# Performance work log

Measured on AMD Instinct MI355X. Metric: run time of the kernel, lower is better.

Reference implementation:

```python
import jax, jax.numpy as jnp
import numpy as np

H, D, TS, A, R, TR = 256, 2, 32, 4, 16, 8  # h_size, max_output_degree, t_size, n_aggr, rank, t_rank
BS = 16384


def setup_inputs() -> dict:
    key = jax.random.key(0)
    ks = jax.random.split(key, 9)
    return {
        "neighbour_h": jax.random.normal(ks[0], (BS, D, H), jnp.float32),
        "type_embs": jax.random.normal(ks[1], (BS, TS), jnp.float32),
        # per-child input projections U: (max_output_degree, n_aggr, h_size, rank)
        "U": jax.random.normal(ks[2], (D, A, H, R), jnp.float32) * 0.05,
        "b": jax.random.normal(ks[3], (D, A, 1, R), jnp.float32) * 0.05,
        # type projection
        "U_type": jax.random.normal(ks[4], (TS, A * TR), jnp.float32) * 0.05,
        "b_type": jax.random.normal(ks[5], (1, A * TR), jnp.float32) * 0.05,
        # stacked augmented core tensors T_list: (n_aggr, t_rank+1, rank+1, rank+1, rank)
        "T": jax.random.normal(ks[6], (A, TR + 1, R + 1, R + 1, R), jnp.float32) * 0.02,
        # output projection
        "U_output": jax.random.normal(ks[7], (A, R, H), jnp.float32) * 0.05,
        "b_output": jax.random.normal(ks[8], (A, 1, H), jnp.float32) * 0.05,
    }


def _aug(x):
    # append a constant-1 feature along the last dim: (bs, a, d) -> (bs, a, d+1)
    bs, a, _ = x.shape
    return jnp.concatenate([x, jnp.ones((bs, a, 1), x.dtype)], axis=-1)


def reference(neighbour_h, type_embs, U, b, U_type, b_type, T, U_output, b_output):
    # child projections: (bs, n_ch, n_aggr, rank)
    ch = jnp.einsum('bch,cahr->bcar', neighbour_h, U) + b[:, :, 0, :]
    # type projection: (bs, n_aggr, t_rank)
    tp = (type_embs @ U_type + b_type).reshape(-1, A, TR)
    # augmented (homogeneous) inputs
    h0 = _aug(tp)         # (bs, a, TR+1)
    h1 = _aug(ch[:, 0])   # (bs, a, R+1)
    h2 = _aug(ch[:, 1])   # (bs, a, R+1)
    # sequential multilinear (Tucker/HOSVD) contraction with the core tensor,
    # vectorized over batch and aggregators (original loops over n_aggr)
    r = jnp.einsum('bap,apqrs->baqrs', h0, T)
    r = jnp.einsum('baq,baqrs->bars', h1, r)
    g = jnp.einsum('bar,bars->bas', h2, r)            # (bs, a, R)
    out = jnp.einsum('bar,arh->bah', g, U_output) + b_output[:, 0, :]
    return out.reshape(neighbour_h.shape[0], -1)      # (bs, n_aggr*h_size)
```

## Files before the change

### kernel.cpp

```cpp
#include <hip/hip_runtime.h>

#define NTHR 512
#define TB 32

typedef __attribute__((ext_vector_type(8))) short bf16x8;
typedef __attribute__((ext_vector_type(4))) float f32x4;
typedef float4 f4;
typedef unsigned short u16;

__device__ __forceinline__ u16 f2b(float x) {
  union { float f; unsigned u; } v; v.f = x;
  unsigned r = (v.u + 0x7fffu + ((v.u >> 16) & 1u)) >> 16;
  return (u16)r;
}
__device__ __forceinline__ float b2f(u16 u) {
  union { unsigned u; float f; } v; v.u = ((unsigned)u) << 16;
  return v.f;
}
__device__ __forceinline__ unsigned pack2(float a, float b) {
  return (unsigned)f2b(a) | ((unsigned)f2b(b) << 16);
}
__device__ __forceinline__ unsigned cvtpk(float lo, float hi) {
  unsigned r;
  asm("v_cvt_pk_bf16_f32 %0, %1, %2" : "=v"(r) : "v"(lo), "v"(hi));
  return r;
}

extern "C" __global__ void hosvd_prep(const float* __restrict__ U,
                                      const float* __restrict__ T,
                                      const float* __restrict__ UO,
                                      unsigned* __restrict__ ws32) {
  int id = blockIdx.x * 256 + threadIdx.x;
  if (id < 92160) {
    int j2 = id & 3, frag = id >> 2;
    int l = frag & 63, f2 = frag >> 6;
    int p = f2 % 9, akt = f2 / 9;
    int kt = akt % 10, a = akt / 10;
    int s = l & 15;
    float v[2];
    #pragma unroll
    for (int j = 0; j < 2; ++j) {
      int kp = kt * 32 + (l >> 4) * 8 + j2 * 2 + j;
      float x = 0.f;
      if (kp < 306) {
        int q = (unsigned)kp / 18u, r = kp - q * 18;
        if (r < 17) x = T[(((a * 9 + p) * 17 + q) * 17 + r) * 16 + s];
      }
      v[j] = x;
    }
    ws32[id] = pack2(v[0], v[1]);
  } else if (id < 108544) {
    int rel = id - 92160;
    int j2 = rel & 3, frag = rel >> 2;
    int l = frag & 63, f2 = frag >> 6;
    int kt = f2 & 7, g = f2 >> 3;
    int a = g & 3, c = g >> 2;
    int rr = l & 15;
    int k = kt * 32 + (l >> 4) * 8 + j2 * 2;
    float v0 = U[((c * 4 + a) * 256 + k + 0) * 16 + rr];
    float v1 = U[((c * 4 + a) * 256 + k + 1) * 16 + rr];
    ws32[id] = pack2(v0, v1);
  } else if (id < 124928) {
    int rel = id - 108544;
    int j2 = rel & 3, frag = rel >> 2;
    int l = frag & 63, f2 = frag >> 6;
    int ht = f2 & 15, a = f2 >> 4;
    int h = ht * 16 + (l & 15);
    int k = (l >> 4) * 8 + j2 * 2;
    float v0 = (k + 0 < 16) ? UO[(a * 16 + k + 0) * 256 + h] : 0.f;
    float v1 = (k + 1 < 16) ? UO[(a * 16 + k + 1) * 256 + h] : 0.f;
    ws32[id] = pack2(v0, v1);
  }
}

#define MFMA_B(A, B, C) __builtin_amdgcn_mfma_f32_16x16x32_bf16(A, B, C, 0, 0, 0)

extern "C" __global__ __launch_bounds__(NTHR, 4)
void hosvd_main(const float* __restrict__ nh, const float* __restrict__ te,
                const float* __restrict__ bw, const float* __restrict__ Ut,
                const float* __restrict__ bt, const float* __restrict__ bO,
                const u16* __restrict__ BTf, const u16* __restrict__ UcTf,
                const u16* __restrict__ UOTf, float* __restrict__ out) {
  __shared__ __align__(16) u16   s_u[18688];
  __shared__ __align__(16) u16   s_ch[TB * 164];
  __shared__ __align__(16) float s_tpt[36 * 32];
  __shared__ __align__(16) u16   s_g[TB * 136];

  const int t = threadIdx.x;
  const int ib0 = blockIdx.x * TB;
  const int w = t >> 6, l = t & 63;
  const int rl = l & 15, q = l >> 4;

  float* teL = (float*)s_g;
  float* UtL = (float*)&s_u[16640];

  if (t < 256) {
    const int row = t >> 3, cc = (t >> 2) & 1, aa = t & 3;
    *(uint2*)&s_ch[row * 164 + cc * 80 + aa * 20 + 16] = make_uint2(0x3F80u, 0u);
  }
  if (t < 128) {
    const int aa = t >> 5, row = t & 31;
    s_tpt[(aa * 9 + 8) * 32 + row] = 1.0f;
  }

  if (t < 256) {
    const int row = t >> 3, k4 = t & 7;
    f4 v = *(const f4*)&te[(size_t)(ib0 + row) * 32 + k4 * 4];
    float* d = &teL[row * 33 + k4 * 4];
    d[0] = v.x; d[1] = v.y; d[2] = v.z; d[3] = v.w;
  } else {
    const int j = t - 256;
    *(f4*)&UtL[j * 4] = *(const f4*)&Ut[j * 4];
  }
  for (int lp = t; lp < 4096; lp += NTHR) {
    const int row = lp >> 7, rem = lp & 127;
    const int c = rem >> 6, k0 = (rem & 63) * 4;
    f4 v = *(const f4*)&nh[((size_t)(ib0 + row) * 2 + c) * 256 + k0];
    *(uint2*)&s_u[row * 520 + c * 256 + k0] =
        make_uint2(cvtpk(v.x, v.y), cvtpk(v.z, v.w));
  }
  __syncthreads();

  {
    const int i = t >> 4, o = t & 15;
    const int off = o * 2;
    const int aa = off >> 3, p0 = off & 7;
    float acc0 = bt[off], acc1 = bt[off + 1];
    #pragma unroll
    for (int k = 0; k < 32; ++k) {
      float tv = teL[i * 33 + k];
      float2 u = *(const float2*)&UtL[k * 32 + off];
      acc0 = fmaf(tv, u.x, acc0);
      acc1 = fmaf(tv, u.y, acc1);
    }
    s_tpt[(aa * 9 + p0) * 32 + i]     = acc0;
    s_tpt[(aa * 9 + p0 + 1) * 32 + i] = acc1;
  }

  {
    const int c = w >> 2, a = w & 3;
    const u16* u0 = &UcTf[((size_t)((c * 4 + a) * 8) * 64 + l) * 8];
    bf16x8 C0 = *(const bf16x8*)(u0 + 0 * 512);
    bf16x8 C1 = *(const bf16x8*)(u0 + 1 * 512);
    bf16x8 C2 = *(const bf16x8*)(u0 + 2 * 512);
    bf16x8 C3 = *(const bf16x8*)(u0 + 3 * 512);
    bf16x8 C4 = *(const bf16x8*)(u0 + 4 * 512);
    bf16x8 C5 = *(const bf16x8*)(u0 + 5 * 512);
    bf16x8 C6 = *(const bf16x8*)(u0 + 6 * 512);
    bf16x8 C7 = *(const bf16x8*)(u0 + 7 * 512);
    f32x4 ac0 = {0.f, 0.f, 0.f, 0.f}, ac1 = {0.f, 0.f, 0.f, 0.f};
    #define PCKT(KT, CB)                                                          \
    {                                                                             \
      bf16x8 A0_ = *(const bf16x8*)&s_u[rl * 520 + c * 256 + KT * 32 + 8 * q];    \
      bf16x8 A1_ = *(const bf16x8*)&s_u[(16 + rl) * 520 + c * 256 + KT * 32 + 8 * q]; \
      ac0 = MFMA_B(A0_, CB, ac0);                                                 \
      ac1 = MFMA_B(A1_, CB, ac1);                                                 \
    }
    PCKT(0, C0) PCKT(1, C1) PCKT(2, C2) PCKT(3, C3)
    PCKT(4, C4) PCKT(5, C5) PCKT(6, C6) PCKT(7, C7)
    #undef PCKT
    const float bias = bw[(c * 4 + a) * 16 + rl];
    #pragma unroll
    for (int reg = 0; reg < 4; ++reg) {
      s_ch[(4 * q + reg) * 164 + c * 80 + a * 20 + rl]      = f2b(ac0[reg] + bias);
      s_ch[(16 + 4 * q + reg) * 164 + c * 80 + a * 20 + rl] = f2b(ac1[reg] + bias);
    }
  }
  __syncthreads();

  {
    const int a = w & 3, m = w >> 2;
    const int row = m * 16 + rl;
    const u16* h1g = &s_ch[row * 164 + a * 20];
    const u16* h2g = &s_ch[row * 164 + 80 + a * 20];

    f32x4 acc[9];
    #pragma unroll
    for (int p = 0; p < 9; ++p) acc[p] = (f32x4){0.f, 0.f, 0.f, 0.f};

    __builtin_amdgcn_s_setprio(1);
    #pragma unroll
    for (int kt = 0; kt < 10; ++kt) {
      const u16* bp = &BTf[(size_t)((a * 10 + kt) * 9) * 512 + l * 8];
      bf16x8 B0 = *(const bf16x8*)(bp + 0 * 512);
      bf16x8 B1 = *(const bf16x8*)(bp + 1 * 512);
      bf16x8 B2 = *(const bf16x8*)(bp + 2 * 512);
      bf16x8 B3 = *(const bf16x8*)(bp + 3 * 512);
      bf16x8 B4 = *(const bf16x8*)(bp + 4 * 512);
      bf16x8 B5 = *(const bf16x8*)(bp + 5 * 512);
      bf16x8 B6 = *(const bf16x8*)(bp + 6 * 512);
      bf16x8 B7 = *(const bf16x8*)(bp + 7 * 512);
      bf16x8 B8 = *(const bf16x8*)(bp + 8 * 512);

      const int k0 = kt * 32 + 8 * q;
      const unsigned qq0 = (unsigned)k0 / 18u;
      const int rr0 = k0 - (int)qq0 * 18;
      const int brk = 18 - rr0;
      const float h1a = b2f(h1g[qq0]);
      const float h1b = b2f(h1g[qq0 + 1]);
      float hv[8];
      #pragma unroll
      for (int j = 0; j < 8; ++j) {
        int rr = rr0 + j;
        rr = (rr >= 18) ? rr - 18 : rr;
        const float h2v = b2f(h2g[rr]);
        const float h1v = (j < brk) ? h1a : h1b;
        hv[j] = h1v * h2v;
      }
      union { unsigned u[4]; bf16x8 v; } Au;
      Au.u[0] = cvtpk(hv[0], hv[1]);
      Au.u[1] = cvtpk(hv[2], hv[3]);
      Au.u[2] = cvtpk(hv[4], hv[5]);
      Au.u[3] = cvtpk(hv[6], hv[7]);

      acc[0] = MFMA_B(Au.v, B0, acc[0]);
      acc[1] = MFMA_B(Au.v, B1, acc[1]);
      acc[2] = MFMA_B(Au.v, B2, acc[2]);
      acc[3] = MFMA_B(Au.v, B3, acc[3]);
      acc[4] = MFMA_B(Au.v, B4, acc[4]);
      acc[5] = MFMA_B(Au.v, B5, acc[5]);
      acc[6] = MFMA_B(Au.v, B6, acc[6]);
      acc[7] = MFMA_B(Au.v, B7, acc[7]);
      acc[8] = MFMA_B(Au.v, B8, acc[8]);
    }
    __builtin_amdgcn_s_setprio(0);

    float gp[4] = {0.f, 0.f, 0.f, 0.f};
    #pragma unroll
    for (int p = 0; p < 9; ++p) {
      f4 tv = *(const f4*)&s_tpt[(a * 9 + p) * 32 + m * 16 + 4 * q];
      gp[0] = fmaf(tv.x, acc[p][0], gp[0]);
      gp[1] = fmaf(tv.y, acc[p][1], gp[1]);
      gp[2] = fmaf(tv.z, acc[p][2], gp[2]);
      gp[3] = fmaf(tv.w, acc[p][3], gp[3]);
    }
    #pragma unroll
    for (int reg = 0; reg < 4; ++reg) {
      const int row2 = m * 16 + 4 * q + reg;
      s_g[row2 * 136 + a * 32 + rl]      = f2b(gp[reg]);
      s_g[row2 * 136 + a * 32 + 16 + rl] = 0;
    }
  }
  __syncthreads();

  {
    const int e = w;
    #pragma unroll
    for (int a = 0; a < 4; ++a) {
      const u16* ub = &UOTf[((size_t)(a * 16 + e * 2) * 64 + l) * 8];
      bf16x8 E0 = *(const bf16x8*)(ub);
      bf16x8 E1 = *(const bf16x8*)(ub + 512);
      bf16x8 A0 = *(const bf16x8*)&s_g[rl * 136 + a * 32 + 8 * q];
      bf16x8 A1 = *(const bf16x8*)&s_g[(16 + rl) * 136 + a * 32 + 8 * q];
      const float b0 = bO[a * 256 + (e * 2 + 0) * 16 + rl];
      const float b1 = bO[a * 256 + (e * 2 + 1) * 16 + rl];
      f32x4 e00 = {b0, b0, b0, b0}, e01 = e00;
      f32x4 e10 = {b1, b1, b1, b1}, e11 = e10;
      e00 = MFMA_B(A0, E0, e00);
      e01 = MFMA_B(A1, E0, e01);
      e10 = MFMA_B(A0, E1, e10);
      e11 = MFMA_B(A1, E1, e11);
      #pragma unroll
      for (int reg = 0; reg < 4; ++reg) {
        const size_t r0 = (size_t)(ib0 + 4 * q + reg) * 1024 + a * 256;
        const size_t r1 = (size_t)(ib0 + 16 + 4 * q + reg) * 1024 + a * 256;
        out[r0 + (e * 2 + 0) * 16 + rl] = e00[reg];
        out[r1 + (e * 2 + 0) * 16 + rl] = e01[reg];
        out[r0 + (e * 2 + 1) * 16 + rl] = e10[reg];
        out[r1 + (e * 2 + 1) * 16 + rl] = e11[reg];
      }
    }
  }
}

extern "C" void kernel_launch(void* const* d_in, const int* in_sizes, int n_in,
                              void* d_out, int out_size, void* d_ws, size_t ws_size,
                              hipStream_t stream) {
  const float* nh = (const float*)d_in[0];
  const float* te = (const float*)d_in[1];
  const float* U  = (const float*)d_in[2];
  const float* bw = (const float*)d_in[3];
  const float* Ut = (const float*)d_in[4];
  const float* bt = (const float*)d_in[5];
  const float* T  = (const float*)d_in[6];
  const float* UO = (const float*)d_in[7];
  const float* bO = (const float*)d_in[8];
  float* out = (float*)d_out;

  unsigned* ws32 = (unsigned*)d_ws;
  hipLaunchKernelGGL(hosvd_prep, dim3(488), dim3(256), 0, stream, U, T, UO, ws32);

  const u16* BTf  = (const u16*)d_ws;
  const u16* UcTf = BTf + 184320;
  const u16* UOTf = UcTf + 32768;

  const int bs = in_sizes[0] / 512;
  hipLaunchKernelGGL(hosvd_main, dim3(bs / TB), dim3(NTHR), 0, stream,
                     nh, te, bw, Ut, bt, bO, BTf, UcTf, UOTf, out);
}
```

Before: 41.49 us.

## Switch all GEMM stages to 32x32x16 MFMA with split-K core contraction

Re-lays out the prepared weight fragments for the 32x32x16 bf16 MFMA shape and rewrites the child projection, core-tensor contraction and output projection to use it. The core contraction now splits K across two wave groups and reduces the partial sums through shared memory plus a lane shuffle. The child projection runs on four waves while the other four compute the type projection concurrently. The intent is fewer MFMA issues and better operand reuse per instruction. In exchange it adds zero-padding work on the N dimension (the last tile uses the padded p index), an extra fp32 reduction through LDS, and larger shared memory use.

```diff
diff --git a/kernel.cpp b/kernel.cpp
--- a/kernel.cpp
+++ b/kernel.cpp
@@ -4,7 +4,7 @@
 #define TB 32
 
 typedef __attribute__((ext_vector_type(8))) short bf16x8;
-typedef __attribute__((ext_vector_type(4))) float f32x4;
+typedef __attribute__((ext_vector_type(16))) float f32x16;
 typedef float4 f4;
 typedef unsigned short u16;
 
@@ -25,55 +25,55 @@
   asm("v_cvt_pk_bf16_f32 %0, %1, %2" : "=v"(r) : "v"(lo), "v"(hi));
   return r;
 }
+
+#define MFMA32(A, B, C) __builtin_amdgcn_mfma_f32_32x32x16_bf16(A, B, C, 0, 0, 0)
 
 extern "C" __global__ void hosvd_prep(const float* __restrict__ U,
                                       const float* __restrict__ T,
                                       const float* __restrict__ UO,
                                       unsigned* __restrict__ ws32) {
   int id = blockIdx.x * 256 + threadIdx.x;
-  if (id < 92160) {
+  if (id < 102400) {
     int j2 = id & 3, frag = id >> 2;
     int l = frag & 63, f2 = frag >> 6;
-    int p = f2 % 9, akt = f2 / 9;
-    int kt = akt % 10, a = akt / 10;
-    int s = l & 15;
+    int nt = f2 % 5, aks = f2 / 5;
+    int ks = aks % 20, a = aks / 20;
+    int n = nt * 32 + (l & 31);
+    int p = n >> 4, s = n & 15;
     float v[2];
     #pragma unroll
     for (int j = 0; j < 2; ++j) {
-      int kp = kt * 32 + (l >> 4) * 8 + j2 * 2 + j;
+      int kp = ks * 16 + (l >> 5) * 8 + j2 * 2 + j;
+      int q = (unsigned)kp / 18u, r = kp - q * 18;
       float x = 0.f;
-      if (kp < 306) {
-        int q = (unsigned)kp / 18u, r = kp - q * 18;
-        if (r < 17) x = T[(((a * 9 + p) * 17 + q) * 17 + r) * 16 + s];
-      }
+      if (p <= 8 && q <= 16 && r <= 16)
+        x = T[(((a * 9 + p) * 17 + q) * 17 + r) * 16 + s];
       v[j] = x;
     }
     ws32[id] = pack2(v[0], v[1]);
-  } else if (id < 108544) {
-    int rel = id - 92160;
+  } else if (id < 118784) {
+    int rel = id - 102400;
     int j2 = rel & 3, frag = rel >> 2;
     int l = frag & 63, f2 = frag >> 6;
-    int kt = f2 & 7, g = f2 >> 3;
-    int a = g & 3, c = g >> 2;
-    int rr = l & 15;
-    int k = kt * 32 + (l >> 4) * 8 + j2 * 2;
+    int nt = f2 & 1, ks = (f2 >> 1) & 15, c = f2 >> 5;
+    int n = nt * 32 + (l & 31);
+    int a = n >> 4, rr = n & 15;
+    int k = ks * 16 + (l >> 5) * 8 + j2 * 2;
     float v0 = U[((c * 4 + a) * 256 + k + 0) * 16 + rr];
     float v1 = U[((c * 4 + a) * 256 + k + 1) * 16 + rr];
     ws32[id] = pack2(v0, v1);
-  } else if (id < 124928) {
-    int rel = id - 108544;
+  } else if (id < 126976) {
+    int rel = id - 118784;
     int j2 = rel & 3, frag = rel >> 2;
     int l = frag & 63, f2 = frag >> 6;
-    int ht = f2 & 15, a = f2 >> 4;
-    int h = ht * 16 + (l & 15);
-    int k = (l >> 4) * 8 + j2 * 2;
-    float v0 = (k + 0 < 16) ? UO[(a * 16 + k + 0) * 256 + h] : 0.f;
-    float v1 = (k + 1 < 16) ? UO[(a * 16 + k + 1) * 256 + h] : 0.f;
+    int ht = f2 & 7, a = f2 >> 3;
+    int h = ht * 32 + (l & 31);
+    int k = (l >> 5) * 8 + j2 * 2;
+    float v0 = UO[(a * 16 + k + 0) * 256 + h];
+    float v1 = UO[(a * 16 + k + 1) * 256 + h];
     ws32[id] = pack2(v0, v1);
   }
 }
-
-#define MFMA_B(A, B, C) __builtin_amdgcn_mfma_f32_16x16x32_bf16(A, B, C, 0, 0, 0)
 
 extern "C" __global__ __launch_bounds__(NTHR, 4)
 void hosvd_main(const float* __restrict__ nh, const float* __restrict__ te,
@@ -81,18 +81,18 @@
                 const float* __restrict__ bt, const float* __restrict__ bO,
                 const u16* __restrict__ BTf, const u16* __restrict__ UcTf,
                 const u16* __restrict__ UOTf, float* __restrict__ out) {
-  __shared__ __align__(16) u16   s_u[18688];
+  __shared__ __align__(16) u16   s_u[20800];
   __shared__ __align__(16) u16   s_ch[TB * 164];
   __shared__ __align__(16) float s_tpt[36 * 32];
-  __shared__ __align__(16) u16   s_g[TB * 136];
 
   const int t = threadIdx.x;
   const int ib0 = blockIdx.x * TB;
   const int w = t >> 6, l = t & 63;
-  const int rl = l & 15, q = l >> 4;
-
-  float* teL = (float*)s_g;
+  const int l31 = l & 31, hi = l >> 5;
+
   float* UtL = (float*)&s_u[16640];
+  float* teL = (float*)&s_u[18688];
+  float* s_redf = (float*)s_u;
 
   if (t < 256) {
     const int row = t >> 3, cc = (t >> 2) & 1, aa = t & 3;
@@ -121,91 +121,82 @@
   }
   __syncthreads();
 
+  if (w < 4) {
+    const int c = w & 1, nt2 = w >> 1;
+    f32x16 accC = {0.f, 0.f, 0.f, 0.f, 0.f, 0.f, 0.f, 0.f,
+                   0.f, 0.f, 0.f, 0.f, 0.f, 0.f, 0.f, 0.f};
+    #pragma unroll
+    for (int ks = 0; ks < 16; ++ks) {
+      bf16x8 Av = *(const bf16x8*)&s_u[l31 * 520 + c * 256 + ks * 16 + hi * 8];
+      bf16x8 Bv = *(const bf16x8*)
+          &UcTf[(size_t)(((c * 16 + ks) * 2 + nt2) * 64 + l) * 8];
+      accC = MFMA32(Av, Bv, accC);
+    }
+    const int n = nt2 * 32 + l31;
+    const int ca = n >> 4, rr = n & 15;
+    const float bias = bw[(c * 4 + ca) * 16 + rr];
+    #pragma unroll
+    for (int reg = 0; reg < 16; ++reg) {
+      const int row = (reg & 3) + 8 * (reg >> 2) + 4 * hi;
+      s_ch[row * 164 + c * 80 + ca * 20 + rr] = f2b(accC[reg] + bias);
+    }
+  } else {
+    const int t2 = t - 256;
+    const int i = t2 >> 3, off = (t2 & 7) * 4;
+    float ac0 = bt[off], ac1 = bt[off + 1], ac2 = bt[off + 2], ac3 = bt[off + 3];
+    #pragma unroll
+    for (int k = 0; k < 32; ++k) {
+      const float tv = teL[i * 33 + k];
+      f4 u = *(const f4*)&UtL[k * 32 + off];
+      ac0 = fmaf(tv, u.x, ac0);
+      ac1 = fmaf(tv, u.y, ac1);
+      ac2 = fmaf(tv, u.z, ac2);
+      ac3 = fmaf(tv, u.w, ac3);
+    }
+    #pragma unroll
+    for (int jj = 0; jj < 4; ++jj) {
+      const int o2 = off + jj;
+      const float v = (jj == 0) ? ac0 : (jj == 1) ? ac1 : (jj == 2) ? ac2 : ac3;
+      s_tpt[((o2 >> 3) * 9 + (o2 & 7)) * 32 + i] = v;
+    }
+  }
+  __syncthreads();
+
   {
-    const int i = t >> 4, o = t & 15;
-    const int off = o * 2;
-    const int aa = off >> 3, p0 = off & 7;
-    float acc0 = bt[off], acc1 = bt[off + 1];
-    #pragma unroll
-    for (int k = 0; k < 32; ++k) {
-      float tv = teL[i * 33 + k];
-      float2 u = *(const float2*)&UtL[k * 32 + off];
-      acc0 = fmaf(tv, u.x, acc0);
-      acc1 = fmaf(tv, u.y, acc1);
-    }
-    s_tpt[(aa * 9 + p0) * 32 + i]     = acc0;
-    s_tpt[(aa * 9 + p0 + 1) * 32 + i] = acc1;
-  }
-
-  {
-    const int c = w >> 2, a = w & 3;
-    const u16* u0 = &UcTf[((size_t)((c * 4 + a) * 8) * 64 + l) * 8];
-    bf16x8 C0 = *(const bf16x8*)(u0 + 0 * 512);
-    bf16x8 C1 = *(const bf16x8*)(u0 + 1 * 512);
-    bf16x8 C2 = *(const bf16x8*)(u0 + 2 * 512);
-    bf16x8 C3 = *(const bf16x8*)(u0 + 3 * 512);
-    bf16x8 C4 = *(const bf16x8*)(u0 + 4 * 512);
-    bf16x8 C5 = *(const bf16x8*)(u0 + 5 * 512);
-    bf16x8 C6 = *(const bf16x8*)(u0 + 6 * 512);
-    bf16x8 C7 = *(const bf16x8*)(u0 + 7 * 512);
-    f32x4 ac0 = {0.f, 0.f, 0.f, 0.f}, ac1 = {0.f, 0.f, 0.f, 0.f};
-    #define PCKT(KT, CB)                                                          \
-    {                                                                             \
-      bf16x8 A0_ = *(const bf16x8*)&s_u[rl * 520 + c * 256 + KT * 32 + 8 * q];    \
-      bf16x8 A1_ = *(const bf16x8*)&s_u[(16 + rl) * 520 + c * 256 + KT * 32 + 8 * q]; \
-      ac0 = MFMA_B(A0_, CB, ac0);                                                 \
-      ac1 = MFMA_B(A1_, CB, ac1);                                                 \
-    }
-    PCKT(0, C0) PCKT(1, C1) PCKT(2, C2) PCKT(3, C3)
-    PCKT(4, C4) PCKT(5, C5) PCKT(6, C6) PCKT(7, C7)
-    #undef PCKT
-    const float bias = bw[(c * 4 + a) * 16 + rl];
-    #pragma unroll
-    for (int reg = 0; reg < 4; ++reg) {
-      s_ch[(4 * q + reg) * 164 + c * 80 + a * 20 + rl]      = f2b(ac0[reg] + bias);
-      s_ch[(16 + 4 * q + reg) * 164 + c * 80 + a * 20 + rl] = f2b(ac1[reg] + bias);
-    }
-  }
-  __syncthreads();
-
-  {
-    const int a = w & 3, m = w >> 2;
-    const int row = m * 16 + rl;
-    const u16* h1g = &s_ch[row * 164 + a * 20];
-    const u16* h2g = &s_ch[row * 164 + 80 + a * 20];
-
-    f32x4 acc[9];
-    #pragma unroll
-    for (int p = 0; p < 9; ++p) acc[p] = (f32x4){0.f, 0.f, 0.f, 0.f};
+    const int a = w & 3, kh = w >> 2;
+    const u16* h1g = &s_ch[l31 * 164 + a * 20];
+    const u16* h2g = h1g + 80;
+
+    f32x16 acc[5];
+    #pragma unroll
+    for (int nt = 0; nt < 5; ++nt)
+      acc[nt] = (f32x16){0.f, 0.f, 0.f, 0.f, 0.f, 0.f, 0.f, 0.f,
+                         0.f, 0.f, 0.f, 0.f, 0.f, 0.f, 0.f, 0.f};
 
     __builtin_amdgcn_s_setprio(1);
     #pragma unroll
-    for (int kt = 0; kt < 10; ++kt) {
-      const u16* bp = &BTf[(size_t)((a * 10 + kt) * 9) * 512 + l * 8];
+    for (int ks2 = 0; ks2 < 10; ++ks2) {
+      const int ks = kh * 10 + ks2;
+      const u16* bp = &BTf[(size_t)((a * 20 + ks) * 5) * 512 + l * 8];
       bf16x8 B0 = *(const bf16x8*)(bp + 0 * 512);
       bf16x8 B1 = *(const bf16x8*)(bp + 1 * 512);
       bf16x8 B2 = *(const bf16x8*)(bp + 2 * 512);
       bf16x8 B3 = *(const bf16x8*)(bp + 3 * 512);
       bf16x8 B4 = *(const bf16x8*)(bp + 4 * 512);
-      bf16x8 B5 = *(const bf16x8*)(bp + 5 * 512);
-      bf16x8 B6 = *(const bf16x8*)(bp + 6 * 512);
-      bf16x8 B7 = *(const bf16x8*)(bp + 7 * 512);
-      bf16x8 B8 = *(const bf16x8*)(bp + 8 * 512);
-
-      const int k0 = kt * 32 + 8 * q;
-      const unsigned qq0 = (unsigned)k0 / 18u;
-      const int rr0 = k0 - (int)qq0 * 18;
-      const int brk = 18 - rr0;
-      const float h1a = b2f(h1g[qq0]);
-      const float h1b = b2f(h1g[qq0 + 1]);
+
+      const int k0 = ks * 16 + hi * 8;
+      const unsigned q0 = (unsigned)k0 / 18u;
+      const int r0 = k0 - (int)q0 * 18;
+      const int brk = 18 - r0;
+      const float h1a = b2f(h1g[q0]);
+      const float h1b = b2f(h1g[q0 + 1]);
       float hv[8];
       #pragma unroll
       for (int j = 0; j < 8; ++j) {
-        int rr = rr0 + j;
+        int rr = r0 + j;
         rr = (rr >= 18) ? rr - 18 : rr;
         const float h2v = b2f(h2g[rr]);
-        const float h1v = (j < brk) ? h1a : h1b;
-        hv[j] = h1v * h2v;
+        hv[j] = ((j < brk) ? h1a : h1b) * h2v;
       }
       union { unsigned u[4]; bf16x8 v; } Au;
       Au.u[0] = cvtpk(hv[0], hv[1]);
@@ -213,61 +204,79 @@
       Au.u[2] = cvtpk(hv[4], hv[5]);
       Au.u[3] = cvtpk(hv[6], hv[7]);
 
-      acc[0] = MFMA_B(Au.v, B0, acc[0]);
-      acc[1] = MFMA_B(Au.v, B1, acc[1]);
-      acc[2] = MFMA_B(Au.v, B2, acc[2]);
-      acc[3] = MFMA_B(Au.v, B3, acc[3]);
-      acc[4] = MFMA_B(Au.v, B4, acc[4]);
-      acc[5] = MFMA_B(Au.v, B5, acc[5]);
-      acc[6] = MFMA_B(Au.v, B6, acc[6]);
-      acc[7] = MFMA_B(Au.v, B7, acc[7]);
-      acc[8] = MFMA_B(Au.v, B8, acc[8]);
+      acc[0] = MFMA32(Au.v, B0, acc[0]);
+      acc[1] = MFMA32(Au.v, B1, acc[1]);
+      acc[2] = MFMA32(Au.v, B2, acc[2]);
+      acc[3] = MFMA32(Au.v, B3, acc[3]);
+      acc[4] = MFMA32(Au.v, B4, acc[4]);
     }
     __builtin_amdgcn_s_setprio(0);
 
-    float gp[4] = {0.f, 0.f, 0.f, 0.f};
-    #pragma unroll
-    for (int p = 0; p < 9; ++p) {
-      f4 tv = *(const f4*)&s_tpt[(a * 9 + p) * 32 + m * 16 + 4 * q];
-      gp[0] = fmaf(tv.x, acc[p][0], gp[0]);
-      gp[1] = fmaf(tv.y, acc[p][1], gp[1]);
-      gp[2] = fmaf(tv.z, acc[p][2], gp[2]);
-      gp[3] = fmaf(tv.w, acc[p][3], gp[3]);
-    }
-    #pragma unroll
-    for (int reg = 0; reg < 4; ++reg) {
-      const int row2 = m * 16 + 4 * q + reg;
-      s_g[row2 * 136 + a * 32 + rl]      = f2b(gp[reg]);
-      s_g[row2 * 136 + a * 32 + 16 + rl] = 0;
+    float gp[16];
+    #pragma unroll
+    for (int reg = 0; reg < 16; ++reg) gp[reg] = 0.f;
+    #pragma unroll
+    for (int nt = 0; nt < 5; ++nt) {
+      int pp = nt * 2 + (l31 >> 4);
+      if (pp > 8) pp = 8;
+      const float* tpb = &s_tpt[(a * 9 + pp) * 32 + 4 * hi];
+      f4 t0 = *(const f4*)&tpb[0];
+      f4 t1 = *(const f4*)&tpb[8];
+      f4 t2 = *(const f4*)&tpb[16];
+      f4 t3 = *(const f4*)&tpb[24];
+      gp[0]  = fmaf(t0.x, acc[nt][0],  gp[0]);
+      gp[1]  = fmaf(t0.y, acc[nt][1],  gp[1]);
+      gp[2]  = fmaf(t0.z, acc[nt][2],  gp[2]);
+      gp[3]  = fmaf(t0.w, acc[nt][3],  gp[3]);
+      gp[4]  = fmaf(t1.x, acc[nt][4],  gp[4]);
+      gp[5]  = fmaf(t1.y, acc[nt][5],  gp[5]);
+      gp[6]  = fmaf(t1.z, acc[nt][6],  gp[6]);
+      gp[7]  = fmaf(t1.w, acc[nt][7],  gp[7]);
+      gp[8]  = fmaf(t2.x, acc[nt][8],  gp[8]);
+      gp[9]  = fmaf(t2.y, acc[nt][9],  gp[9]);
+      gp[10] = fmaf(t2.z, acc[nt][10], gp[10]);
+      gp[11] = fmaf(t2.w, acc[nt][11], gp[11]);
+      gp[12] = fmaf(t3.x, acc[nt][12], gp[12]);
+      gp[13] = fmaf(t3.y, acc[nt][13], gp[13]);
+      gp[14] = fmaf(t3.z, acc[nt][14], gp[14]);
+      gp[15] = fmaf(t3.w, acc[nt][15], gp[15]);
+    }
+    #pragma unroll
+    for (int reg = 0; reg < 16; ++reg)
+      gp[reg] += __shfl_xor(gp[reg], 16, 64);
+    if ((l & 16) == 0) {
+      const int s = l & 15;
+      #pragma unroll
+      for (int reg = 0; reg < 16; ++reg) {
+        const int row = (reg & 3) + 8 * (reg >> 2) + 4 * hi;
+        s_redf[((kh * 4 + a) * 32 + row) * 16 + s] = gp[reg];
+      }
     }
   }
   __syncthreads();
 
   {
-    const int e = w;
     #pragma unroll
     for (int a = 0; a < 4; ++a) {
-      const u16* ub = &UOTf[((size_t)(a * 16 + e * 2) * 64 + l) * 8];
-      bf16x8 E0 = *(const bf16x8*)(ub);
-      bf16x8 E1 = *(const bf16x8*)(ub + 512);
-      bf16x8 A0 = *(const bf16x8*)&s_g[rl * 136 + a * 32 + 8 * q];
-      bf16x8 A1 = *(const bf16x8*)&s_g[(16 + rl) * 136 + a * 32 + 8 * q];
-      const float b0 = bO[a * 256 + (e * 2 + 0) * 16 + rl];
-      const float b1 = bO[a * 256 + (e * 2 + 1) * 16 + rl];
-      f32x4 e00 = {b0, b0, b0, b0}, e01 = e00;
-      f32x4 e10 = {b1, b1, b1, b1}, e11 = e10;
-      e00 = MFMA_B(A0, E0, e00);
-      e01 = MFMA_B(A1, E0, e01);
-      e10 = MFMA_B(A0, E1, e10);
-      e11 = MFMA_B(A1, E1, e11);
+      const float* r0p = &s_redf[((0 + a) * 32 + l31) * 16 + hi * 8];
+      const float* r1p = &s_redf[((4 + a) * 32 + l31) * 16 + hi * 8];
+      f4 xa = *(const f4*)&r0p[0], xb = *(const f4*)&r0p[4];
+      f4 ya = *(const f4*)&r1p[0], yb = *(const f4*)&r1p[4];
+      union { unsigned u[4]; bf16x8 v; } Au;
+      Au.u[0] = cvtpk(xa.x + ya.x, xa.y + ya.y);
+      Au.u[1] = cvtpk(xa.z + ya.z, xa.w + ya.w);
+      Au.u[2] = cvtpk(xb.x + yb.x, xb.y + yb.y);
+      Au.u[3] = cvtpk(xb.z + yb.z, xb.w + yb.w);
+      bf16x8 Bv = *(const bf16x8*)&UOTf[((size_t)(a * 8 + w) * 64 + l) * 8];
+      const int h = w * 32 + l31;
+      const float bias = bO[a * 256 + h];
+      f32x16 accE = {bias, bias, bias, bias, bias, bias, bias, bias,
+                     bias, bias, bias, bias, bias, bias, bias, bias};
+      accE = MFMA32(Au.v, Bv, accE);
       #pragma unroll
-      for (int reg = 0; reg < 4; ++reg) {
-        const size_t r0 = (size_t)(ib0 + 4 * q + reg) * 1024 + a * 256;
-        const size_t r1 = (size_t)(ib0 + 16 + 4 * q + reg) * 1024 + a * 256;
-        out[r0 + (e * 2 + 0) * 16 + rl] = e00[reg];
-        out[r1 + (e * 2 + 0) * 16 + rl] = e01[reg];
-        out[r0 + (e * 2 + 1) * 16 + rl] = e10[reg];
-        out[r1 + (e * 2 + 1) * 16 + rl] = e11[reg];
+      for (int reg = 0; reg < 16; ++reg) {
+        const int row = (reg & 3) + 8 * (reg >> 2) + 4 * hi;
+        out[(size_t)(ib0 + row) * 1024 + a * 256 + h] = accE[reg];
       }
     }
   }
@@ -288,10 +297,10 @@
   float* out = (float*)d_out;
 
   unsigned* ws32 = (unsigned*)d_ws;
-  hipLaunchKernelGGL(hosvd_prep, dim3(488), dim3(256), 0, stream, U, T, UO, ws32);
+  hipLaunchKernelGGL(hosvd_prep, dim3(496), dim3(256), 0, stream, U, T, UO, ws32);
 
   const u16* BTf  = (const u16*)d_ws;
-  const u16* UcTf = BTf + 184320;
+  const u16* UcTf = BTf + 204800;
   const u16* UOTf = UcTf + 32768;
 
   const int bs = in_sizes[0] / 512;
```

After: 39.47 us. -4.9%, faster.

## Halve block tile to 16 rows with 256 threads and overlap type projection

Applied to the files above, without the earlier changes.

Shrinks the per-block batch tile from 32 to 16 rows with 256 threads, doubling the grid and cutting LDS use per block so more blocks can be resident. The child projection now runs on two warps, each covering four aggregators with its A fragments held in registers, while the other two warps compute the type projection at the same time. Every warp now handles one aggregator for all 16 rows. Each block reloads the core and projection weights, so weight traffic from global/L2 doubles for the same amount of output.

```diff
diff --git a/kernel.cpp b/kernel.cpp
--- a/kernel.cpp
+++ b/kernel.cpp
@@ -1,7 +1,7 @@
 #include <hip/hip_runtime.h>
 
-#define NTHR 512
-#define TB 32
+#define NTHR 256
+#define TB 16
 
 typedef __attribute__((ext_vector_type(8))) short bf16x8;
 typedef __attribute__((ext_vector_type(4))) float f32x4;
@@ -25,6 +25,8 @@
   asm("v_cvt_pk_bf16_f32 %0, %1, %2" : "=v"(r) : "v"(lo), "v"(hi));
   return r;
 }
+
+#define MFMA_B(A, B, C) __builtin_amdgcn_mfma_f32_16x16x32_bf16(A, B, C, 0, 0, 0)
 
 extern "C" __global__ void hosvd_prep(const float* __restrict__ U,
                                       const float* __restrict__ T,
@@ -73,17 +75,15 @@
   }
 }
 
-#define MFMA_B(A, B, C) __builtin_amdgcn_mfma_f32_16x16x32_bf16(A, B, C, 0, 0, 0)
-
 extern "C" __global__ __launch_bounds__(NTHR, 4)
 void hosvd_main(const float* __restrict__ nh, const float* __restrict__ te,
                 const float* __restrict__ bw, const float* __restrict__ Ut,
                 const float* __restrict__ bt, const float* __restrict__ bO,
                 const u16* __restrict__ BTf, const u16* __restrict__ UcTf,
                 const u16* __restrict__ UOTf, float* __restrict__ out) {
-  __shared__ __align__(16) u16   s_u[18688];
+  __shared__ __align__(16) u16   s_u[11424];
   __shared__ __align__(16) u16   s_ch[TB * 164];
-  __shared__ __align__(16) float s_tpt[36 * 32];
+  __shared__ __align__(16) float s_tpt[36 * 16];
   __shared__ __align__(16) u16   s_g[TB * 136];
 
   const int t = threadIdx.x;
@@ -91,28 +91,26 @@
   const int w = t >> 6, l = t & 63;
   const int rl = l & 15, q = l >> 4;
 
-  float* teL = (float*)s_g;
-  float* UtL = (float*)&s_u[16640];
-
-  if (t < 256) {
+  float* UtL = (float*)&s_u[8320];
+  float* teL = (float*)&s_u[10368];
+
+  if (t < 128) {
     const int row = t >> 3, cc = (t >> 2) & 1, aa = t & 3;
     *(uint2*)&s_ch[row * 164 + cc * 80 + aa * 20 + 16] = make_uint2(0x3F80u, 0u);
   }
+  if (t < 64) {
+    const int aa = t >> 4, row = t & 15;
+    s_tpt[(aa * 9 + 8) * 16 + row] = 1.0f;
+  }
+
   if (t < 128) {
-    const int aa = t >> 5, row = t & 31;
-    s_tpt[(aa * 9 + 8) * 32 + row] = 1.0f;
-  }
-
-  if (t < 256) {
     const int row = t >> 3, k4 = t & 7;
     f4 v = *(const f4*)&te[(size_t)(ib0 + row) * 32 + k4 * 4];
     float* d = &teL[row * 33 + k4 * 4];
     d[0] = v.x; d[1] = v.y; d[2] = v.z; d[3] = v.w;
-  } else {
-    const int j = t - 256;
-    *(f4*)&UtL[j * 4] = *(const f4*)&Ut[j * 4];
-  }
-  for (int lp = t; lp < 4096; lp += NTHR) {
+  }
+  *(f4*)&UtL[t * 4] = *(const f4*)&Ut[t * 4];
+  for (int lp = t; lp < 2048; lp += NTHR) {
     const int row = lp >> 7, rem = lp & 127;
     const int c = rem >> 6, k0 = (rem & 63) * 4;
     f4 v = *(const f4*)&nh[((size_t)(ib0 + row) * 2 + c) * 256 + k0];
@@ -121,58 +119,52 @@
   }
   __syncthreads();
 
+  if (w < 2) {
+    const int c = w;
+    bf16x8 Af[8];
+    #pragma unroll
+    for (int kt = 0; kt < 8; ++kt)
+      Af[kt] = *(const bf16x8*)&s_u[rl * 520 + c * 256 + kt * 32 + 8 * q];
+    #pragma unroll
+    for (int a = 0; a < 4; ++a) {
+      const u16* u0 = &UcTf[((size_t)((c * 4 + a) * 8) * 64 + l) * 8];
+      f32x4 ac = {0.f, 0.f, 0.f, 0.f};
+      #pragma unroll
+      for (int kt = 0; kt < 8; ++kt) {
+        bf16x8 Bv = *(const bf16x8*)(u0 + kt * 512);
+        ac = MFMA_B(Af[kt], Bv, ac);
+      }
+      const float bias = bw[(c * 4 + a) * 16 + rl];
+      #pragma unroll
+      for (int reg = 0; reg < 4; ++reg)
+        s_ch[(4 * q + reg) * 164 + c * 80 + a * 20 + rl] = f2b(ac[reg] + bias);
+    }
+  } else {
+    const int t2 = t - 128;
+    const int i = t2 >> 3, off = (t2 & 7) * 4;
+    float ac0 = bt[off], ac1 = bt[off + 1], ac2 = bt[off + 2], ac3 = bt[off + 3];
+    #pragma unroll
+    for (int k = 0; k < 32; ++k) {
+      const float tv = teL[i * 33 + k];
+      f4 u = *(const f4*)&UtL[k * 32 + off];
+      ac0 = fmaf(tv, u.x, ac0);
+      ac1 = fmaf(tv, u.y, ac1);
+      ac2 = fmaf(tv, u.z, ac2);
+      ac3 = fmaf(tv, u.w, ac3);
+    }
+    #pragma unroll
+    for (int jj = 0; jj < 4; ++jj) {
+      const int o2 = off + jj;
+      const float v = (jj == 0) ? ac0 : (jj == 1) ? ac1 : (jj == 2) ? ac2 : ac3;
+      s_tpt[((o2 >> 3) * 9 + (o2 & 7)) * 16 + i] = v;
+    }
+  }
+  __syncthreads();
+
   {
-    const int i = t >> 4, o = t & 15;
-    const int off = o * 2;
-    const int aa = off >> 3, p0 = off & 7;
-    float acc0 = bt[off], acc1 = bt[off + 1];
-    #pragma unroll
-    for (int k = 0; k < 32; ++k) {
-      float tv = teL[i * 33 + k];
-      float2 u = *(const float2*)&UtL[k * 32 + off];
-      acc0 = fmaf(tv, u.x, acc0);
-      acc1 = fmaf(tv, u.y, acc1);
-    }
-    s_tpt[(aa * 9 + p0) * 32 + i]     = acc0;
-    s_tpt[(aa * 9 + p0 + 1) * 32 + i] = acc1;
-  }
-
-  {
-    const int c = w >> 2, a = w & 3;
-    const u16* u0 = &UcTf[((size_t)((c * 4 + a) * 8) * 64 + l) * 8];
-    bf16x8 C0 = *(const bf16x8*)(u0 + 0 * 512);
-    bf16x8 C1 = *(const bf16x8*)(u0 + 1 * 512);
-    bf16x8 C2 = *(const bf16x8*)(u0 + 2 * 512);
-    bf16x8 C3 = *(const bf16x8*)(u0 + 3 * 512);
-    bf16x8 C4 = *(const bf16x8*)(u0 + 4 * 512);
-    bf16x8 C5 = *(const bf16x8*)(u0 + 5 * 512);
-    bf16x8 C6 = *(const bf16x8*)(u0 + 6 * 512);
-    bf16x8 C7 = *(const bf16x8*)(u0 + 7 * 512);
-    f32x4 ac0 = {0.f, 0.f, 0.f, 0.f}, ac1 = {0.f, 0.f, 0.f, 0.f};
-    #define PCKT(KT, CB)                                                          \
-    {                                                                             \
-      bf16x8 A0_ = *(const bf16x8*)&s_u[rl * 520 + c * 256 + KT * 32 + 8 * q];    \
-      bf16x8 A1_ = *(const bf16x8*)&s_u[(16 + rl) * 520 + c * 256 + KT * 32 + 8 * q]; \
-      ac0 = MFMA_B(A0_, CB, ac0);                                                 \
-      ac1 = MFMA_B(A1_, CB, ac1);                                                 \
-    }
-    PCKT(0, C0) PCKT(1, C1) PCKT(2, C2) PCKT(3, C3)
-    PCKT(4, C4) PCKT(5, C5) PCKT(6, C6) PCKT(7, C7)
-    #undef PCKT
-    const float bias = bw[(c * 4 + a) * 16 + rl];
-    #pragma unroll
-    for (int reg = 0; reg < 4; ++reg) {
-      s_ch[(4 * q + reg) * 164 + c * 80 + a * 20 + rl]      = f2b(ac0[reg] + bias);
-      s_ch[(16 + 4 * q + reg) * 164 + c * 80 + a * 20 + rl] = f2b(ac1[reg] + bias);
-    }
-  }
-  __syncthreads();
-
-  {
-    const int a = w & 3, m = w >> 2;
-    const int row = m * 16 + rl;
-    const u16* h1g = &s_ch[row * 164 + a * 20];
-    const u16* h2g = &s_ch[row * 164 + 80 + a * 20];
+    const int a = w;
+    const u16* h1g = &s_ch[rl * 164 + a * 20];
+    const u16* h2g = h1g + 80;
 
     f32x4 acc[9];
     #pragma unroll
@@ -193,19 +185,18 @@
       bf16x8 B8 = *(const bf16x8*)(bp + 8 * 512);
 
       const int k0 = kt * 32 + 8 * q;
-      const unsigned qq0 = (unsigned)k0 / 18u;
-      const int rr0 = k0 - (int)qq0 * 18;
-      const int brk = 18 - rr0;
-      const float h1a = b2f(h1g[qq0]);
-      const float h1b = b2f(h1g[qq0 + 1]);
+      const unsigned q0 = (unsigned)k0 / 18u;
+      const int r0 = k0 - (int)q0 * 18;
+      const int brk = 18 - r0;
+      const float h1a = b2f(h1g[q0]);
+      const float h1b = b2f(h1g[q0 + 1]);
       float hv[8];
       #pragma unroll
       for (int j = 0; j < 8; ++j) {
-        int rr = rr0 + j;
+        int rr = r0 + j;
         rr = (rr >= 18) ? rr - 18 : rr;
         const float h2v = b2f(h2g[rr]);
-        const float h1v = (j < brk) ? h1a : h1b;
-        hv[j] = h1v * h2v;
+        hv[j] = ((j < brk) ? h1a : h1b) * h2v;
       }
       union { unsigned u[4]; bf16x8 v; } Au;
       Au.u[0] = cvtpk(hv[0], hv[1]);
@@ -228,7 +219,7 @@
     float gp[4] = {0.f, 0.f, 0.f, 0.f};
     #pragma unroll
     for (int p = 0; p < 9; ++p) {
-      f4 tv = *(const f4*)&s_tpt[(a * 9 + p) * 32 + m * 16 + 4 * q];
+      f4 tv = *(const f4*)&s_tpt[(a * 9 + p) * 16 + 4 * q];
       gp[0] = fmaf(tv.x, acc[p][0], gp[0]);
       gp[1] = fmaf(tv.y, acc[p][1], gp[1]);
       gp[2] = fmaf(tv.z, acc[p][2], gp[2]);
@@ -236,7 +227,7 @@
     }
     #pragma unroll
     for (int reg = 0; reg < 4; ++reg) {
-      const int row2 = m * 16 + 4 * q + reg;
+      const int row2 = 4 * q + reg;
       s_g[row2 * 136 + a * 32 + rl]      = f2b(gp[reg]);
       s_g[row2 * 136 + a * 32 + 16 + rl] = 0;
     }
@@ -247,27 +238,18 @@
     const int e = w;
     #pragma unroll
     for (int a = 0; a < 4; ++a) {
-      const u16* ub = &UOTf[((size_t)(a * 16 + e * 2) * 64 + l) * 8];
-      bf16x8 E0 = *(const bf16x8*)(ub);
-      bf16x8 E1 = *(const bf16x8*)(ub + 512);
-      bf16x8 A0 = *(const bf16x8*)&s_g[rl * 136 + a * 32 + 8 * q];
-      bf16x8 A1 = *(const bf16x8*)&s_g[(16 + rl) * 136 + a * 32 + 8 * q];
-      const float b0 = bO[a * 256 + (e * 2 + 0) * 16 + rl];
-      const float b1 = bO[a * 256 + (e * 2 + 1) * 16 + rl];
-      f32x4 e00 = {b0, b0, b0, b0}, e01 = e00;
-      f32x4 e10 = {b1, b1, b1, b1}, e11 = e10;
-      e00 = MFMA_B(A0, E0, e00);
-      e01 = MFMA_B(A1, E0, e01);
-      e10 = MFMA_B(A0, E1, e10);
-      e11 = MFMA_B(A1, E1, e11);
-      #pragma unroll
-      for (int reg = 0; reg < 4; ++reg) {
-        const size_t r0 = (size_t)(ib0 + 4 * q + reg) * 1024 + a * 256;
-        const size_t r1 = (size_t)(ib0 + 16 + 4 * q + reg) * 1024 + a * 256;
-        out[r0 + (e * 2 + 0) * 16 + rl] = e00[reg];
-        out[r1 + (e * 2 + 0) * 16 + rl] = e01[reg];
-        out[r0 + (e * 2 + 1) * 16 + rl] = e10[reg];
-        out[r1 + (e * 2 + 1) * 16 + rl] = e11[reg];
+      bf16x8 A = *(const bf16x8*)&s_g[rl * 136 + a * 32 + 8 * q];
+      #pragma unroll
+      for (int j = 0; j < 4; ++j) {
+        const int ht = e * 4 + j;
+        bf16x8 Bv = *(const bf16x8*)&UOTf[((size_t)(a * 16 + ht) * 64 + l) * 8];
+        const float bias = bO[a * 256 + ht * 16 + rl];
+        f32x4 accE = {bias, bias, bias, bias};
+        accE = MFMA_B(A, Bv, accE);
+        #pragma unroll
+        for (int reg = 0; reg < 4; ++reg)
+          out[(size_t)(ib0 + 4 * q + reg) * 1024 + a * 256 + ht * 16 + rl] =
+              accE[reg];
       }
     }
   }
```

New measurement: 42.07 us. No clear change (+1.4%).
